# Performance work log

Hardware: AMD Instinct MI355X
Metric: run time of the kernel (lower is better)

Reference implementation:

```python
import jax, jax.numpy as jnp
import numpy as np


def setup_inputs() -> dict:
    key = jax.random.key(0)
    k1, k2 = jax.random.split(key)
    # [batch, seq, in_features] activations
    x = jax.random.normal(k1, (4, 4096, 2048), dtype=jnp.float32)
    # fp32 master weight [out_features, in_features]; quantized inside reference
    weight = jax.random.normal(k2, (2048, 2048), dtype=jnp.float32) * 0.02
    return {"x": x, "weight": weight}


def reference(x, weight):
    num_bits = 8
    Qn = -(2 ** (num_bits - 1))       # -128
    Qp = 2 ** (num_bits - 1) - 1      # 127

    # Per-row absmax int8 activation quantization (activation_quant)
    si = Qp / jnp.clip(jnp.max(jnp.abs(x), axis=-1, keepdims=True), 1e-5)  # [B,S,1]
    qx = jnp.clip(jnp.round(x * si), Qn, Qp)  # int8 values held in fp32 (exact)

    # Ternary weight quantization (weight_quant): sw scalar = 1/mean|W|
    sw = 1.0 / jnp.clip(jnp.mean(jnp.abs(weight)), 1e-5)
    qw = jnp.clip(jnp.round(weight * sw), -1.0, 1.0)  # {-1,0,1}

    acc = jnp.einsum("bsk,nk->bsn", qx, qw)  # [B,S,out]

    # post_quant_process: dequantize by si and sw, cast to half
    out = ((acc / si) / sw).astype(jnp.float16)
    return out
```

## Files before the change

### kernel.cpp

```cpp
#include <hip/hip_runtime.h>

#define K_DIM 2048
#define N_DIM 2048
#define M_DIM 16384

typedef int v4i __attribute__((ext_vector_type(4)));
typedef int v16i __attribute__((ext_vector_type(16)));


__device__ __forceinline__ void lds16(const void* g, void* l) {
    __builtin_amdgcn_global_load_lds(
        (const __attribute__((address_space(1))) unsigned int*)g,
        (__attribute__((address_space(3))) unsigned int*)l,
        16, 0, 0);
}

__global__ __launch_bounds__(256) void k_wsum(const float* __restrict__ w,
                                              double* __restrict__ part) {
    int tid = blockIdx.x * 256 + threadIdx.x;
    int stride = gridDim.x * 256;
    const float4* w4 = (const float4*)w;
    double s = 0.0;
    for (int i = tid; i < (N_DIM * K_DIM / 4); i += stride) {
        float4 v = w4[i];
        s += (double)fabsf(v.x);
        s += (double)fabsf(v.y);
        s += (double)fabsf(v.z);
        s += (double)fabsf(v.w);
    }
#pragma unroll
    for (int off = 32; off; off >>= 1) s += __shfl_xor(s, off, 64);
    __shared__ double sp[4];
    int lane = threadIdx.x & 63, wv = threadIdx.x >> 6;
    if (lane == 0) sp[wv] = s;
    __syncthreads();
    if (threadIdx.x == 0) part[blockIdx.x] = sp[0] + sp[1] + sp[2] + sp[3];
}

__global__ __launch_bounds__(256) void k_wred(const double* __restrict__ part,
                                              float* __restrict__ invsw_out) {
    double s = part[threadIdx.x];
#pragma unroll
    for (int off = 32; off; off >>= 1) s += __shfl_xor(s, off, 64);
    __shared__ double sp[4];
    int lane = threadIdx.x & 63, wv = threadIdx.x >> 6;
    if (lane == 0) sp[wv] = s;
    __syncthreads();
    if (threadIdx.x == 0) {
        double total = sp[0] + sp[1] + sp[2] + sp[3];
        float mean = (float)(total * (1.0 / (double)(N_DIM * K_DIM)));
        *invsw_out = fmaxf(mean, 1e-5f);
    }
}

__global__ __launch_bounds__(256) void k_quant_w(const float* __restrict__ w,
                                                 signed char* __restrict__ qw,
                                                 const float* __restrict__ invsw_p) {
    float sw = 1.0f / (*invsw_p);
    int tid = blockIdx.x * 256 + threadIdx.x;
    float4 v = ((const float4*)w)[tid];
    int q0 = (int)fminf(fmaxf(rintf(v.x * sw), -1.f), 1.f);
    int q1 = (int)fminf(fmaxf(rintf(v.y * sw), -1.f), 1.f);
    int q2 = (int)fminf(fmaxf(rintf(v.z * sw), -1.f), 1.f);
    int q3 = (int)fminf(fmaxf(rintf(v.w * sw), -1.f), 1.f);
    ((int*)qw)[tid] = (q0 & 255) | ((q1 & 255) << 8) | ((q2 & 255) << 16) | ((q3 & 255) << 24);
}

__global__ __launch_bounds__(256) void k_quant_x(const float* __restrict__ x,
                                                 signed char* __restrict__ qx,
                                                 float* __restrict__ si_out) {
    int row = blockIdx.x * 4 + (threadIdx.x >> 6);
    int lane = threadIdx.x & 63;
    const float4* xr = (const float4*)(x + (size_t)row * K_DIM);
    float4 v[8];
    float mx = 0.f;
#pragma unroll
    for (int c = 0; c < 8; c++) {
        v[c] = xr[c * 64 + lane];
        mx = fmaxf(mx, fmaxf(fmaxf(fabsf(v[c].x), fabsf(v[c].y)),
                             fmaxf(fabsf(v[c].z), fabsf(v[c].w))));
    }
#pragma unroll
    for (int off = 32; off; off >>= 1) mx = fmaxf(mx, __shfl_xor(mx, off, 64));
    float si = 127.0f / fmaxf(mx, 1e-5f);
    if (lane == 0) si_out[row] = si;
    int* qr = (int*)(qx + (size_t)row * K_DIM);
#pragma unroll
    for (int c = 0; c < 8; c++) {
        int q0 = (int)fminf(fmaxf(rintf(v[c].x * si), -128.f), 127.f);
        int q1 = (int)fminf(fmaxf(rintf(v[c].y * si), -128.f), 127.f);
        int q2 = (int)fminf(fmaxf(rintf(v[c].z * si), -128.f), 127.f);
        int q3 = (int)fminf(fmaxf(rintf(v[c].w * si), -128.f), 127.f);
        qr[c * 64 + lane] = (q0 & 255) | ((q1 & 255) << 8) | ((q2 & 255) << 16) | ((q3 & 255) << 24);
    }
}

__global__ __launch_bounds__(256, 2) void k_gemm(const signed char* __restrict__ qx,
                                                 const signed char* __restrict__ qw,
                                                 const float* __restrict__ si,
                                                 const float* __restrict__ invsw_p,
                                                 float* __restrict__ out) {
    __shared__ __align__(16) signed char As[16384];
    __shared__ __align__(16) signed char Bs[8192];
    const int t = threadIdx.x;
    const int lane = t & 63, wv = t >> 6;
    const int wr = wv >> 1, wc = wv & 1;
    const int l31 = lane & 31, lh = lane >> 5;
    const int bn = blockIdx.x, bm = blockIdx.y;

    const signed char* aG = qx + (size_t)(bm * 256 + t) * K_DIM;
    const signed char* bG = qw + (size_t)(bn * 128 + (t & 127)) * K_DIM + ((t >> 7) << 4);
    const int t16 = t << 4;

    v16i acc[4][2] = {};

    for (int k0 = 0; k0 < K_DIM; k0 += 64) {
        lds16(aG + k0,      As + t16);
        lds16(aG + k0 + 16, As + 4096 + t16);
        lds16(aG + k0 + 32, As + 8192 + t16);
        lds16(aG + k0 + 48, As + 12288 + t16);
        lds16(bG + k0,      Bs + t16);
        lds16(bG + k0 + 32, Bs + 4096 + t16);
        __syncthreads();

#pragma unroll
        for (int ks = 0; ks < 2; ks++) {
            v4i af[4], bf[2];
#pragma unroll
            for (int mt = 0; mt < 4; mt++)
                af[mt] = *(const v4i*)(As + (((ks * 2 + lh) * 256 + wr * 128 + mt * 32 + l31) << 4));
#pragma unroll
            for (int nt = 0; nt < 2; nt++)
                bf[nt] = *(const v4i*)(Bs + (((ks * 2 + lh) * 128 + wc * 64 + nt * 32 + l31) << 4));
#pragma unroll
            for (int mt = 0; mt < 4; mt++)
#pragma unroll
                for (int nt = 0; nt < 2; nt++)
                    acc[mt][nt] = __builtin_amdgcn_mfma_i32_32x32x32_i8(af[mt], bf[nt], acc[mt][nt], 0, 0, 0);
        }
        __syncthreads();
    }

    float invsw = *invsw_p;
#pragma unroll
    for (int mt = 0; mt < 4; mt++) {
        int rowb = bm * 256 + wr * 128 + mt * 32 + (lh << 2);
        float sc[16];
#pragma unroll
        for (int r = 0; r < 16; r++)
            sc[r] = invsw / si[rowb + (r & 3) + ((r >> 2) << 3)];
#pragma unroll
        for (int nt = 0; nt < 2; nt++) {
            int col = bn * 128 + wc * 64 + nt * 32 + l31;
#pragma unroll
            for (int r = 0; r < 16; r++) {
                int row = rowb + (r & 3) + ((r >> 2) << 3);
                float vv = (float)acc[mt][nt][r] * sc[r];
                out[(size_t)row * N_DIM + col] = (float)(_Float16)vv;
            }
        }
    }
}

extern "C" void kernel_launch(void* const* d_in, const int* in_sizes, int n_in,
                              void* d_out, int out_size, void* d_ws, size_t ws_size,
                              hipStream_t stream) {
    const float* x = (const float*)d_in[0];
    const float* w = (const float*)d_in[1];
    float* out = (float*)d_out;
    char* ws = (char*)d_ws;

    double* part = (double*)ws;
    float* invsw = (float*)(ws + 2048);
    float* si = (float*)(ws + 4096);
    signed char* qw = (signed char*)(ws + 4096 + 65536);
    signed char* qx = qw + (size_t)N_DIM * K_DIM;

    k_wsum<<<256, 256, 0, stream>>>(w, part);
    k_wred<<<1, 256, 0, stream>>>(part, invsw);
    k_quant_x<<<4096, 256, 0, stream>>>(x, qx, si);
    k_quant_w<<<4096, 256, 0, stream>>>(w, qw, invsw);
    k_gemm<<<dim3(N_DIM / 128, M_DIM / 256), 256, 0, stream>>>(qx, qw, si, invsw, out);
}
```

Baseline: 373.6 us.

## Pre-tile quantized operands into GEMM LDS order and fuse weight reduction

The quantize kernels now write int8 activations and ternary weights in a tiled layout that matches the GEMM's shared-memory tile order. Each k-step's global-to-LDS load then reads one contiguous block instead of strided rows. The final weight-sum reduction is folded into the weight quantization kernel, which removes one launch, and every block redoes the small 256-entry reduction. The quantize kernels now do scattered 4-byte stores, which could cost some write efficiency in exchange for coalesced GEMM loads.

Result: faster. 330.4 us (-11.6%).

```diff
diff --git a/kernel.cpp b/kernel.cpp
--- a/kernel.cpp
+++ b/kernel.cpp
@@ -18,10 +18,9 @@
 __global__ __launch_bounds__(256) void k_wsum(const float* __restrict__ w,
                                               double* __restrict__ part) {
     int tid = blockIdx.x * 256 + threadIdx.x;
-    int stride = gridDim.x * 256;
     const float4* w4 = (const float4*)w;
     double s = 0.0;
-    for (int i = tid; i < (N_DIM * K_DIM / 4); i += stride) {
+    for (int i = tid; i < (N_DIM * K_DIM / 4); i += 65536) {
         float4 v = w4[i];
         s += (double)fabsf(v.x);
         s += (double)fabsf(v.y);
@@ -37,37 +36,46 @@
     if (threadIdx.x == 0) part[blockIdx.x] = sp[0] + sp[1] + sp[2] + sp[3];
 }
 
-__global__ __launch_bounds__(256) void k_wred(const double* __restrict__ part,
-                                              float* __restrict__ invsw_out) {
+__global__ __launch_bounds__(256) void k_quant_w(const float* __restrict__ w,
+                                                 signed char* __restrict__ qw_t,
+                                                 const double* __restrict__ part,
+                                                 float* __restrict__ invsw_out) {
     double s = part[threadIdx.x];
 #pragma unroll
     for (int off = 32; off; off >>= 1) s += __shfl_xor(s, off, 64);
     __shared__ double sp[4];
+    __shared__ float s_invsw;
     int lane = threadIdx.x & 63, wv = threadIdx.x >> 6;
     if (lane == 0) sp[wv] = s;
     __syncthreads();
     if (threadIdx.x == 0) {
         double total = sp[0] + sp[1] + sp[2] + sp[3];
         float mean = (float)(total * (1.0 / (double)(N_DIM * K_DIM)));
-        *invsw_out = fmaxf(mean, 1e-5f);
+        s_invsw = fmaxf(mean, 1e-5f);
+        if (blockIdx.x == 0) *invsw_out = s_invsw;
+    }
+    __syncthreads();
+    float sw = 1.0f / s_invsw;
+
+    int row = blockIdx.x * 4 + wv;
+    const float4* wr_ = (const float4*)(w + (size_t)row * K_DIM);
+    int bn = row >> 7, ri = row & 127;
+    signed char* base = qw_t + (size_t)bn * 262144 + (((lane >> 2) & 3) << 11) + (ri << 4) + ((lane & 3) << 2);
+    int ksBase = lane >> 4;
+#pragma unroll
+    for (int c = 0; c < 8; c++) {
+        float4 v = wr_[c * 64 + lane];
+        int q0 = (int)fminf(fmaxf(rintf(v.x * sw), -1.f), 1.f);
+        int q1 = (int)fminf(fmaxf(rintf(v.y * sw), -1.f), 1.f);
+        int q2 = (int)fminf(fmaxf(rintf(v.z * sw), -1.f), 1.f);
+        int q3 = (int)fminf(fmaxf(rintf(v.w * sw), -1.f), 1.f);
+        int q = (q0 & 255) | ((q1 & 255) << 8) | ((q2 & 255) << 16) | ((q3 & 255) << 24);
+        *(int*)(base + (size_t)(4 * c + ksBase) * 8192) = q;
     }
 }
 
-__global__ __launch_bounds__(256) void k_quant_w(const float* __restrict__ w,
-                                                 signed char* __restrict__ qw,
-                                                 const float* __restrict__ invsw_p) {
-    float sw = 1.0f / (*invsw_p);
-    int tid = blockIdx.x * 256 + threadIdx.x;
-    float4 v = ((const float4*)w)[tid];
-    int q0 = (int)fminf(fmaxf(rintf(v.x * sw), -1.f), 1.f);
-    int q1 = (int)fminf(fmaxf(rintf(v.y * sw), -1.f), 1.f);
-    int q2 = (int)fminf(fmaxf(rintf(v.z * sw), -1.f), 1.f);
-    int q3 = (int)fminf(fmaxf(rintf(v.w * sw), -1.f), 1.f);
-    ((int*)qw)[tid] = (q0 & 255) | ((q1 & 255) << 8) | ((q2 & 255) << 16) | ((q3 & 255) << 24);
-}
-
 __global__ __launch_bounds__(256) void k_quant_x(const float* __restrict__ x,
-                                                 signed char* __restrict__ qx,
+                                                 signed char* __restrict__ qx_t,
                                                  float* __restrict__ si_out) {
     int row = blockIdx.x * 4 + (threadIdx.x >> 6);
     int lane = threadIdx.x & 63;
@@ -84,19 +92,23 @@
     for (int off = 32; off; off >>= 1) mx = fmaxf(mx, __shfl_xor(mx, off, 64));
     float si = 127.0f / fmaxf(mx, 1e-5f);
     if (lane == 0) si_out[row] = si;
-    int* qr = (int*)(qx + (size_t)row * K_DIM);
+
+    int bm = row >> 8, ri = row & 255;
+    signed char* base = qx_t + (size_t)bm * 524288 + (((lane >> 2) & 3) << 12) + (ri << 4) + ((lane & 3) << 2);
+    int ksBase = lane >> 4;
 #pragma unroll
     for (int c = 0; c < 8; c++) {
         int q0 = (int)fminf(fmaxf(rintf(v[c].x * si), -128.f), 127.f);
         int q1 = (int)fminf(fmaxf(rintf(v[c].y * si), -128.f), 127.f);
         int q2 = (int)fminf(fmaxf(rintf(v[c].z * si), -128.f), 127.f);
         int q3 = (int)fminf(fmaxf(rintf(v[c].w * si), -128.f), 127.f);
-        qr[c * 64 + lane] = (q0 & 255) | ((q1 & 255) << 8) | ((q2 & 255) << 16) | ((q3 & 255) << 24);
+        int q = (q0 & 255) | ((q1 & 255) << 8) | ((q2 & 255) << 16) | ((q3 & 255) << 24);
+        *(int*)(base + (size_t)(4 * c + ksBase) * 16384) = q;
     }
 }
 
-__global__ __launch_bounds__(256, 2) void k_gemm(const signed char* __restrict__ qx,
-                                                 const signed char* __restrict__ qw,
+__global__ __launch_bounds__(256, 2) void k_gemm(const signed char* __restrict__ qx_t,
+                                                 const signed char* __restrict__ qw_t,
                                                  const float* __restrict__ si,
                                                  const float* __restrict__ invsw_p,
                                                  float* __restrict__ out) {
@@ -108,30 +120,32 @@
     const int l31 = lane & 31, lh = lane >> 5;
     const int bn = blockIdx.x, bm = blockIdx.y;
 
-    const signed char* aG = qx + (size_t)(bm * 256 + t) * K_DIM;
-    const signed char* bG = qw + (size_t)(bn * 128 + (t & 127)) * K_DIM + ((t >> 7) << 4);
+    const signed char* aT = qx_t + (size_t)bm * 524288;
+    const signed char* bT = qw_t + (size_t)bn * 262144;
     const int t16 = t << 4;
 
     v16i acc[4][2] = {};
 
-    for (int k0 = 0; k0 < K_DIM; k0 += 64) {
-        lds16(aG + k0,      As + t16);
-        lds16(aG + k0 + 16, As + 4096 + t16);
-        lds16(aG + k0 + 32, As + 8192 + t16);
-        lds16(aG + k0 + 48, As + 12288 + t16);
-        lds16(bG + k0,      Bs + t16);
-        lds16(bG + k0 + 32, Bs + 4096 + t16);
+    for (int ks = 0; ks < 32; ks++) {
+        const signed char* aS = aT + (ks << 14);
+        const signed char* bS = bT + (ks << 13);
+        lds16(aS + t16,          As + t16);
+        lds16(aS + 4096 + t16,   As + 4096 + t16);
+        lds16(aS + 8192 + t16,   As + 8192 + t16);
+        lds16(aS + 12288 + t16,  As + 12288 + t16);
+        lds16(bS + t16,          Bs + t16);
+        lds16(bS + 4096 + t16,   Bs + 4096 + t16);
         __syncthreads();
 
 #pragma unroll
-        for (int ks = 0; ks < 2; ks++) {
+        for (int ks2 = 0; ks2 < 2; ks2++) {
             v4i af[4], bf[2];
 #pragma unroll
             for (int mt = 0; mt < 4; mt++)
-                af[mt] = *(const v4i*)(As + (((ks * 2 + lh) * 256 + wr * 128 + mt * 32 + l31) << 4));
+                af[mt] = *(const v4i*)(As + (((ks2 * 2 + lh) * 256 + wr * 128 + mt * 32 + l31) << 4));
 #pragma unroll
             for (int nt = 0; nt < 2; nt++)
-                bf[nt] = *(const v4i*)(Bs + (((ks * 2 + lh) * 128 + wc * 64 + nt * 32 + l31) << 4));
+                bf[nt] = *(const v4i*)(Bs + (((ks2 * 2 + lh) * 128 + wc * 64 + nt * 32 + l31) << 4));
 #pragma unroll
             for (int mt = 0; mt < 4; mt++)
 #pragma unroll
@@ -173,12 +187,11 @@
     double* part = (double*)ws;
     float* invsw = (float*)(ws + 2048);
     float* si = (float*)(ws + 4096);
-    signed char* qw = (signed char*)(ws + 4096 + 65536);
-    signed char* qx = qw + (size_t)N_DIM * K_DIM;
+    signed char* qw_t = (signed char*)(ws + 4096 + 65536);
+    signed char* qx_t = qw_t + (size_t)N_DIM * K_DIM;
 
     k_wsum<<<256, 256, 0, stream>>>(w, part);
-    k_wred<<<1, 256, 0, stream>>>(part, invsw);
-    k_quant_x<<<4096, 256, 0, stream>>>(x, qx, si);
-    k_quant_w<<<4096, 256, 0, stream>>>(w, qw, invsw);
-    k_gemm<<<dim3(N_DIM / 128, M_DIM / 256), 256, 0, stream>>>(qx, qw, si, invsw, out);
+    k_quant_x<<<4096, 256, 0, stream>>>(x, qx_t, si);
+    k_quant_w<<<512, 256, 0, stream>>>(w, qw_t, part, invsw);
+    k_gemm<<<dim3(N_DIM / 128, M_DIM / 256), 256, 0, stream>>>(qx_t, qw_t, si, invsw, out);
 }
```
